# Kernel optimization log

Measured on AMD Instinct MI355X. Metric: run time of the kernel, lower is better.

## Reference

```python
import jax, jax.numpy as jnp
import numpy as np

B, S, E, D, DE = 8, 128, 50, 300, 50  # batch, seq, edge_dim, gcn_dim, dep_embed_dim
EPS = 1e-6


def setup_inputs() -> dict:
    key = jax.random.key(0)
    ks = jax.random.split(key, 9)
    weight_prob_softmax = jax.nn.softmax(jax.random.normal(ks[0], (B, S, S, E)), axis=2)
    weight_adj = jax.random.normal(ks[1], (B, S, S, E))
    gcn_inputs = jax.random.normal(ks[2], (B, S, D))
    # self-loop added to adjacency after permute -> [B, E, S, S]; identity loops
    self_loop = jnp.broadcast_to(jnp.eye(S, dtype=jnp.float32), (B, E, S, S))
    W_w = jax.random.normal(ks[3], (D, D)) * 0.05          # gcn linear (in, out)
    W_b = jnp.zeros((D,))
    ln_a = jnp.ones((D,))
    ln_b = jnp.zeros((D,))
    refine_W = jax.random.normal(ks[4], (2 * D + 3 * E, DE)) * 0.05  # (750, 50)
    refine_b = jnp.zeros((DE,))
    return {
        "weight_prob_softmax": weight_prob_softmax,
        "weight_adj": weight_adj,
        "gcn_inputs": gcn_inputs,
        "self_loop": self_loop,
        "W_w": W_w, "W_b": W_b,
        "ln_a": ln_a, "ln_b": ln_b,
        "refine_W": refine_W, "refine_b": refine_b,
    }


def reference(weight_prob_softmax, weight_adj, gcn_inputs, self_loop,
              W_w, W_b, ln_a, ln_b, refine_W, refine_b):
    b, s, d = gcn_inputs.shape
    e = weight_prob_softmax.shape[-1]
    # [B,S,S,E] -> [B,E,S,S], add self loops
    wps = jnp.transpose(weight_prob_softmax, (0, 3, 1, 2)) + self_loop
    # per-relation-channel message passing: Ax[b,e,i,:] = sum_j wps[b,e,i,j] * x[b,j,:]
    Ax = jnp.einsum('beij,bjd->beid', wps, gcn_inputs)
    Ax = Ax.mean(axis=1)  # avg pooling over edge channels -> [B,S,D]
    h = Ax @ W_w + W_b
    # LayerNorm with unbiased std (torch x.std default) and (std + eps)
    mean = h.mean(axis=-1, keepdims=True)
    var_unbiased = jnp.sum((h - mean) ** 2, axis=-1, keepdims=True) / (d - 1)
    std = jnp.sqrt(var_unbiased)
    h = ln_a * (h - mean) / (std + EPS) + ln_b
    node = jax.nn.relu(h)  # [B,S,D]
    # node1[b,i,j] = node[b,j]; node2[b,i,j] = node[b,i]
    node1 = jnp.broadcast_to(node[:, None, :, :], (b, s, s, d))
    node2 = jnp.broadcast_to(node[:, :, None, :], (b, s, s, d))
    # diagonal edge features: [B,E,S] -> [B,S,E]
    diag = jnp.transpose(jnp.diagonal(weight_adj, axis1=1, axis2=2), (0, 2, 1))
    edge_i = jnp.broadcast_to(diag[:, None, :, :], (b, s, s, e))  # edge_i[b,i,j]=diag[b,j]
    edge_j = jnp.broadcast_to(diag[:, :, None, :], (b, s, s, e))  # edge_j[b,i,j]=diag[b,i]
    feat = jnp.concatenate([weight_adj, edge_i, edge_j, node1, node2], axis=-1)
    edge_out = feat @ refine_W + refine_b  # [B,S,S,DE]
    return node, edge_out
```

## Files before the change

### kernel.cpp

```cpp
#include <hip/hip_runtime.h>
#include <hip/hip_bf16.h>


typedef __bf16 bf16x8 __attribute__((ext_vector_type(8)));
typedef float f32x4 __attribute__((ext_vector_type(4)));

__device__ __forceinline__ unsigned short f2bf(float f) {
    __hip_bfloat16 h = __float2bfloat16(f);
    union { __hip_bfloat16 h; unsigned short u; } c; c.h = h; return c.u;
}

__global__ void __launch_bounds__(512) k_node(
    const float* __restrict__ wps,
    const float* __restrict__ wa,
    const float* __restrict__ x,
    const float* __restrict__ Ww,
    const float* __restrict__ Wb,
    const float* __restrict__ lna,
    const float* __restrict__ lnb,
    const float* __restrict__ Rw,
    const float* __restrict__ rb,
    float* __restrict__ node_out,
    float* __restrict__ R1, float* __restrict__ R2)
{
    __shared__ __align__(16) float stageF[12800];
    __shared__ float Ml[4][128];
    __shared__ float axm[4][304];
    __shared__ float hl[4][304];
    __shared__ float diag[4][52];
    __shared__ float stats[8];
    int tid = threadIdx.x;
    int b = blockIdx.x >> 5;
    int ig = blockIdx.x & 31;
    int row0 = b * 128 + ig * 4;

    const float4* wb4 = (const float4*)(wps + (size_t)row0 * 6400);
    float4* s4 = (float4*)stageF;
    for (int c = 0; c < 2; ++c) {
        for (int i4 = tid; i4 < 3200; i4 += 512) s4[i4] = wb4[c * 3200 + i4];
        __syncthreads();
        if (tid < 256) {
            int rl = tid >> 7, j = tid & 127;
            const float* p = stageF + (rl * 128 + j) * 50;
            float s = 0.f;
#pragma unroll
            for (int e = 0; e < 50; e += 2) s += p[e] + p[e + 1];
            int r = c * 2 + rl;
            Ml[r][j] = s * (1.0f / 50.0f) + (((ig * 4 + r) == j) ? 1.0f : 0.0f);
        }
        __syncthreads();
    }
    if (tid < 200) {
        int r = tid / 50, e = tid % 50;
        diag[r][e] = wa[(((size_t)(row0 + r)) * 128 + (ig * 4 + r)) * 50 + e];
    }

    if (tid < 300) {
        float a0 = 0.f, a1 = 0.f, a2 = 0.f, a3 = 0.f;
        const float* xp = x + (size_t)b * 38400 + tid;
#pragma unroll 4
        for (int j = 0; j < 128; ++j) {
            float xv = xp[j * 300];
            a0 += Ml[0][j] * xv; a1 += Ml[1][j] * xv;
            a2 += Ml[2][j] * xv; a3 += Ml[3][j] * xv;
        }
        axm[0][tid] = a0; axm[1][tid] = a1; axm[2][tid] = a2; axm[3][tid] = a3;
    }
    __syncthreads();

    if (tid < 300) {
        float wb = Wb[tid];
        float h0 = wb, h1 = wb, h2 = wb, h3 = wb;
        const float* wp = Ww + tid;
#pragma unroll 4
        for (int k = 0; k < 300; ++k) {
            float w = wp[k * 300];
            h0 += axm[0][k] * w; h1 += axm[1][k] * w;
            h2 += axm[2][k] * w; h3 += axm[3][k] * w;
        }
        hl[0][tid] = h0; hl[1][tid] = h1; hl[2][tid] = h2; hl[3][tid] = h3;
    }
    __syncthreads();

    if (tid < 256) {
        int wv = tid >> 6, lane = tid & 63;
        float s1 = 0.f, s2 = 0.f;
        for (int dd = lane; dd < 300; dd += 64) {
            float v = hl[wv][dd]; s1 += v; s2 += v * v;
        }
        for (int off = 32; off > 0; off >>= 1) {
            s1 += __shfl_down(s1, off);
            s2 += __shfl_down(s2, off);
        }
        if (lane == 0) {
            float mean = s1 * (1.0f / 300.0f);
            float var = (s2 - 300.0f * mean * mean) * (1.0f / 299.0f);
            var = fmaxf(var, 0.0f);
            stats[wv * 2] = mean;
            stats[wv * 2 + 1] = 1.0f / (sqrtf(var) + 1e-6f);
        }
    }
    __syncthreads();
    if (tid < 300) {
        float la = lna[tid], lb = lnb[tid];
#pragma unroll
        for (int r = 0; r < 4; ++r) {
            float v = la * (hl[r][tid] - stats[r * 2]) * stats[r * 2 + 1] + lb;
            v = fmaxf(v, 0.0f);
            node_out[(size_t)(row0 + r) * 300 + tid] = v;
            axm[r][tid] = v;
        }
    }
    __syncthreads();

    if (tid < 400) {
        int k = tid % 50, p = tid / 50;
        float r1a[4] = {0.f, 0.f, 0.f, 0.f};
        float r2a[4] = {0.f, 0.f, 0.f, 0.f};
        int i0 = p * 44, i1 = (i0 + 44 < 350) ? i0 + 44 : 350;
        for (int idx = i0; idx < i1; ++idx) {
            float w1, w2;
            if (idx < 50) { w1 = Rw[(50 + idx) * 50 + k]; w2 = Rw[(100 + idx) * 50 + k]; }
            else { int d = idx - 50; w1 = Rw[(150 + d) * 50 + k]; w2 = Rw[(450 + d) * 50 + k]; }
#pragma unroll
            for (int r = 0; r < 4; ++r) {
                float m = (idx < 50) ? diag[r][idx] : axm[r][idx - 50];
                r1a[r] += m * w1; r2a[r] += m * w2;
            }
        }
#pragma unroll
        for (int r = 0; r < 4; ++r) {
            stageF[p * 200 + r * 50 + k] = r1a[r];
            stageF[1600 + p * 200 + r * 50 + k] = r2a[r];
        }
    }
    __syncthreads();
    if (tid < 200) {
        int r = tid / 50, k = tid % 50;
        float r1 = 0.f, r2 = rb[k];
#pragma unroll
        for (int p = 0; p < 8; ++p) {
            r1 += stageF[p * 200 + r * 50 + k];
            r2 += stageF[1600 + p * 200 + r * 50 + k];
        }
        R1[(size_t)(row0 + r) * 50 + k] = r1;
        R2[(size_t)(row0 + r) * 50 + k] = r2;
    }
}

__global__ void __launch_bounds__(256) k_edge(
    const float* __restrict__ wa,
    const float* __restrict__ Rw,
    const float* __restrict__ R1, const float* __restrict__ R2,
    float* __restrict__ eout)
{
    __shared__ __align__(16) unsigned char smem[27648];
    unsigned short* waA  = (unsigned short*)smem;
    unsigned short* rwBT = (unsigned short*)(smem + 18432);
    float* outF = (float*)smem;
    int tid = threadIdx.x;
    int bi = blockIdx.x;
    int b = bi >> 7;

    for (int idx = tid; idx < 2304; idx += 256) ((unsigned int*)rwBT)[idx] = 0u;
    for (int idx = tid; idx < 1408; idx += 256) {
        int j = idx / 11, c = idx % 11;
        *((unsigned int*)(waA + j * 72 + 50) + c) = 0u;
    }
    __syncthreads();

    const float2* wap = (const float2*)(wa + (size_t)bi * 6400);
    for (int idx = tid; idx < 3200; idx += 256) {
        float2 v = wap[idx];
        int f = idx * 2;
        int j = f / 50, e = f % 50;
        unsigned int pack = (unsigned int)f2bf(v.x) | ((unsigned int)f2bf(v.y) << 16);
        *(unsigned int*)(waA + j * 72 + e) = pack;
    }
    for (int idx = tid; idx < 2500; idx += 256) {
        int e = idx / 50, kk = idx % 50;
        rwBT[kk * 72 + e] = f2bf(Rw[idx]);
    }
    __syncthreads();

    int lane = tid & 63, wv = tid >> 6;
    int q = lane >> 4, lr = lane & 15;
    f32x4 acc[2][4] = {};

#pragma unroll
    for (int ks = 0; ks < 2; ++ks) {
        int e0 = ks * 32 + q * 8;
        bf16x8 a0 = *(const bf16x8*)&waA[(wv * 32 + lr) * 72 + e0];
        bf16x8 a1 = *(const bf16x8*)&waA[(wv * 32 + 16 + lr) * 72 + e0];
#pragma unroll
        for (int nt = 0; nt < 4; ++nt) {
            bf16x8 bb = *(const bf16x8*)&rwBT[(nt * 16 + lr) * 72 + e0];
            acc[0][nt] = __builtin_amdgcn_mfma_f32_16x16x32_bf16(a0, bb, acc[0][nt], 0, 0, 0);
            acc[1][nt] = __builtin_amdgcn_mfma_f32_16x16x32_bf16(a1, bb, acc[1][nt], 0, 0, 0);
        }
    }
    __syncthreads();

    const float* r2p = R2 + (size_t)bi * 50;
#pragma unroll
    for (int nt = 0; nt < 4; ++nt) {
        int kk = nt * 16 + lr;
        if (kk < 50) {
            float r2v = r2p[kk];
#pragma unroll
            for (int mi = 0; mi < 2; ++mi) {
                int jbase = wv * 32 + mi * 16 + q * 4;
#pragma unroll
                for (int r = 0; r < 4; ++r)
                    outF[(jbase + r) * 50 + kk] = acc[mi][nt][r] + r2v;
            }
        }
    }
    __syncthreads();

    const float4* R1b = (const float4*)(R1 + (size_t)b * 6400);
    const float4* L4  = (const float4*)outF;
    float4* op4 = (float4*)(eout + (size_t)bi * 6400);
    for (int f4 = tid; f4 < 1600; f4 += 256) {
        float4 v = L4[f4];
        float4 r = R1b[f4];
        v.x += r.x; v.y += r.y; v.z += r.z; v.w += r.w;
        op4[f4] = v;
    }
}

extern "C" void kernel_launch(void* const* d_in, const int* in_sizes, int n_in,
                              void* d_out, int out_size, void* d_ws, size_t ws_size,
                              hipStream_t stream)
{
    const float* wps = (const float*)d_in[0];
    const float* wa  = (const float*)d_in[1];
    const float* x   = (const float*)d_in[2];
    const float* Ww  = (const float*)d_in[4];
    const float* Wb  = (const float*)d_in[5];
    const float* lna = (const float*)d_in[6];
    const float* lnb = (const float*)d_in[7];
    const float* Rw  = (const float*)d_in[8];
    const float* rb  = (const float*)d_in[9];

    float* R1 = (float*)d_ws;
    float* R2 = ((float*)d_ws) + 51200;

    float* node_out = (float*)d_out;
    float* edge_out = node_out + 307200;

    k_node<<<256, 512, 0, stream>>>(wps, wa, x, Ww, Wb, lna, lnb, Rw, rb,
                                    node_out, R1, R2);
    k_edge<<<1024, 256, 0, stream>>>(wa, Rw, R1, R2, edge_out);
}
```

Baseline: 184.3 us.

## Precompute X·W once per batch and reassociate node aggregation

Reassociates (M·X)·W into M·(X·W): a new kernel computes X·W for all rows once, so each node block only does a 128-length aggregation instead of separate 128- and 300-length matmuls. The per-row edge-channel mean is now read directly from global memory without a shared staging pass, and the diag-dependent refine partial sums are computed by otherwise idle threads alongside the aggregation. It adds a third launch and uses the edge_out buffer as scratch for XW, which is safe only because k_edge overwrites it afterwards.

```diff
diff --git a/kernel.cpp b/kernel.cpp
--- a/kernel.cpp
+++ b/kernel.cpp
@@ -10,11 +10,37 @@
     union { __hip_bfloat16 h; unsigned short u; } c; c.h = h; return c.u;
 }
 
+__global__ void __launch_bounds__(320) k_xw(
+    const float* __restrict__ x, const float* __restrict__ Ww,
+    float* __restrict__ XW)
+{
+    __shared__ __align__(16) float xr[304];
+    int tid = threadIdx.x;
+    int row = blockIdx.x;
+    if (tid < 300) xr[tid] = x[(size_t)row * 300 + tid];
+    else if (tid < 304) xr[tid] = 0.f;
+    __syncthreads();
+    if (tid < 300) {
+        const float* wp = Ww + tid;
+        const f32x4* x4 = (const f32x4*)xr;
+        float acc = 0.f;
+#pragma unroll 5
+        for (int k4 = 0; k4 < 75; ++k4) {
+            f32x4 xv = x4[k4];
+            int k = k4 * 4;
+            acc += xv[0] * wp[(k + 0) * 300];
+            acc += xv[1] * wp[(k + 1) * 300];
+            acc += xv[2] * wp[(k + 2) * 300];
+            acc += xv[3] * wp[(k + 3) * 300];
+        }
+        XW[(size_t)row * 300 + tid] = acc;
+    }
+}
+
 __global__ void __launch_bounds__(512) k_node(
     const float* __restrict__ wps,
     const float* __restrict__ wa,
-    const float* __restrict__ x,
-    const float* __restrict__ Ww,
+    const float* __restrict__ XW,
     const float* __restrict__ Wb,
     const float* __restrict__ lna,
     const float* __restrict__ lnb,
@@ -23,62 +49,63 @@
     float* __restrict__ node_out,
     float* __restrict__ R1, float* __restrict__ R2)
 {
-    __shared__ __align__(16) float stageF[12800];
-    __shared__ float Ml[4][128];
-    __shared__ float axm[4][304];
+    __shared__ __align__(16) float Ml[128][4];
     __shared__ float hl[4][304];
+    __shared__ float nodeL[4][304];
     __shared__ float diag[4][52];
     __shared__ float stats[8];
+    __shared__ float part1[14][200];
+    __shared__ float part2[14][200];
     int tid = threadIdx.x;
     int b = blockIdx.x >> 5;
     int ig = blockIdx.x & 31;
     int row0 = b * 128 + ig * 4;
 
-    const float4* wb4 = (const float4*)(wps + (size_t)row0 * 6400);
-    float4* s4 = (float4*)stageF;
-    for (int c = 0; c < 2; ++c) {
-        for (int i4 = tid; i4 < 3200; i4 += 512) s4[i4] = wb4[c * 3200 + i4];
-        __syncthreads();
-        if (tid < 256) {
-            int rl = tid >> 7, j = tid & 127;
-            const float* p = stageF + (rl * 128 + j) * 50;
-            float s = 0.f;
-#pragma unroll
-            for (int e = 0; e < 50; e += 2) s += p[e] + p[e + 1];
-            int r = c * 2 + rl;
-            Ml[r][j] = s * (1.0f / 50.0f) + (((ig * 4 + r) == j) ? 1.0f : 0.0f);
-        }
-        __syncthreads();
-    }
     if (tid < 200) {
         int r = tid / 50, e = tid % 50;
         diag[r][e] = wa[(((size_t)(row0 + r)) * 128 + (ig * 4 + r)) * 50 + e];
     }
-
-    if (tid < 300) {
-        float a0 = 0.f, a1 = 0.f, a2 = 0.f, a3 = 0.f;
-        const float* xp = x + (size_t)b * 38400 + tid;
-#pragma unroll 4
-        for (int j = 0; j < 128; ++j) {
-            float xv = xp[j * 300];
-            a0 += Ml[0][j] * xv; a1 += Ml[1][j] * xv;
-            a2 += Ml[2][j] * xv; a3 += Ml[3][j] * xv;
-        }
-        axm[0][tid] = a0; axm[1][tid] = a1; axm[2][tid] = a2; axm[3][tid] = a3;
+    {
+        int r = tid >> 7, j = tid & 127;
+        const float2* p = (const float2*)(wps + ((size_t)(row0 + r)) * 6400 + j * 50);
+        float s = 0.f;
+#pragma unroll
+        for (int n = 0; n < 25; ++n) { float2 v = p[n]; s += v.x + v.y; }
+        Ml[j][r] = s * (1.0f / 50.0f) + (((ig * 4 + r) == j) ? 1.0f : 0.0f);
     }
     __syncthreads();
 
     if (tid < 300) {
         float wb = Wb[tid];
         float h0 = wb, h1 = wb, h2 = wb, h3 = wb;
-        const float* wp = Ww + tid;
-#pragma unroll 4
-        for (int k = 0; k < 300; ++k) {
-            float w = wp[k * 300];
-            h0 += axm[0][k] * w; h1 += axm[1][k] * w;
-            h2 += axm[2][k] * w; h3 += axm[3][k] * w;
+        const float* xwp = XW + (size_t)b * 38400 + tid;
+        const f32x4* M4 = (const f32x4*)Ml;
+#pragma unroll 16
+        for (int j = 0; j < 128; ++j) {
+            float xv = xwp[j * 300];
+            f32x4 m = M4[j];
+            h0 += m[0] * xv; h1 += m[1] * xv; h2 += m[2] * xv; h3 += m[3] * xv;
         }
         hl[0][tid] = h0; hl[1][tid] = h1; hl[2][tid] = h2; hl[3][tid] = h3;
+    } else if (tid >= 312) {
+        int t = tid - 312, p = t / 50, k = t % 50;
+        int e0 = p * 13, e1 = (e0 + 13 < 50) ? e0 + 13 : 50;
+        float r1a[4] = {0.f, 0.f, 0.f, 0.f};
+        float r2a[4] = {0.f, 0.f, 0.f, 0.f};
+        for (int e = e0; e < e1; ++e) {
+            float w1 = Rw[(50 + e) * 50 + k];
+            float w2 = Rw[(100 + e) * 50 + k];
+#pragma unroll
+            for (int r = 0; r < 4; ++r) {
+                r1a[r] += diag[r][e] * w1;
+                r2a[r] += diag[r][e] * w2;
+            }
+        }
+#pragma unroll
+        for (int r = 0; r < 4; ++r) {
+            part1[p][r * 50 + k] = r1a[r];
+            part2[p][r * 50 + k] = r2a[r];
+        }
     }
     __syncthreads();
 
@@ -101,6 +128,7 @@
         }
     }
     __syncthreads();
+
     if (tid < 300) {
         float la = lna[tid], lb = lnb[tid];
 #pragma unroll
@@ -108,43 +136,44 @@
             float v = la * (hl[r][tid] - stats[r * 2]) * stats[r * 2 + 1] + lb;
             v = fmaxf(v, 0.0f);
             node_out[(size_t)(row0 + r) * 300 + tid] = v;
-            axm[r][tid] = v;
-        }
-    }
-    __syncthreads();
-
-    if (tid < 400) {
-        int k = tid % 50, p = tid / 50;
+            nodeL[r][tid] = v;
+        }
+    }
+    __syncthreads();
+
+    if (tid < 500) {
+        int p = tid / 50, k = tid % 50;
+        int d0 = p * 30;
         float r1a[4] = {0.f, 0.f, 0.f, 0.f};
         float r2a[4] = {0.f, 0.f, 0.f, 0.f};
-        int i0 = p * 44, i1 = (i0 + 44 < 350) ? i0 + 44 : 350;
-        for (int idx = i0; idx < i1; ++idx) {
-            float w1, w2;
-            if (idx < 50) { w1 = Rw[(50 + idx) * 50 + k]; w2 = Rw[(100 + idx) * 50 + k]; }
-            else { int d = idx - 50; w1 = Rw[(150 + d) * 50 + k]; w2 = Rw[(450 + d) * 50 + k]; }
+#pragma unroll 6
+        for (int d = d0; d < d0 + 30; ++d) {
+            float w1 = Rw[(150 + d) * 50 + k];
+            float w2 = Rw[(450 + d) * 50 + k];
 #pragma unroll
             for (int r = 0; r < 4; ++r) {
-                float m = (idx < 50) ? diag[r][idx] : axm[r][idx - 50];
-                r1a[r] += m * w1; r2a[r] += m * w2;
+                r1a[r] += nodeL[r][d] * w1;
+                r2a[r] += nodeL[r][d] * w2;
             }
         }
 #pragma unroll
         for (int r = 0; r < 4; ++r) {
-            stageF[p * 200 + r * 50 + k] = r1a[r];
-            stageF[1600 + p * 200 + r * 50 + k] = r2a[r];
-        }
-    }
-    __syncthreads();
+            part1[4 + p][r * 50 + k] = r1a[r];
+            part2[4 + p][r * 50 + k] = r2a[r];
+        }
+    }
+    __syncthreads();
+
     if (tid < 200) {
         int r = tid / 50, k = tid % 50;
-        float r1 = 0.f, r2 = rb[k];
-#pragma unroll
-        for (int p = 0; p < 8; ++p) {
-            r1 += stageF[p * 200 + r * 50 + k];
-            r2 += stageF[1600 + p * 200 + r * 50 + k];
-        }
-        R1[(size_t)(row0 + r) * 50 + k] = r1;
-        R2[(size_t)(row0 + r) * 50 + k] = r2;
+        float s1 = 0.f, s2 = rb[k];
+#pragma unroll
+        for (int p = 0; p < 14; ++p) {
+            s1 += part1[p][r * 50 + k];
+            s2 += part2[p][r * 50 + k];
+        }
+        R1[(size_t)(row0 + r) * 50 + k] = s1;
+        R2[(size_t)(row0 + r) * 50 + k] = s2;
     }
 }
 
@@ -248,8 +277,10 @@
 
     float* node_out = (float*)d_out;
     float* edge_out = node_out + 307200;
-
-    k_node<<<256, 512, 0, stream>>>(wps, wa, x, Ww, Wb, lna, lnb, Rw, rb,
+    float* XW = edge_out;
+
+    k_xw  <<<1024, 320, 0, stream>>>(x, Ww, XW);
+    k_node<<<256, 512, 0, stream>>>(wps, wa, XW, Wb, lna, lnb, Rw, rb,
                                     node_out, R1, R2);
     k_edge<<<1024, 256, 0, stream>>>(wa, Rw, R1, R2, edge_out);
 }
```

New measurement: 160.3 us. 1.15x faster.

## Split edge-channel mean into separate kernel and widen node kernel with split-K

Applied to the files above, without the earlier changes.

The channel-mean reduction over the softmax tensor moves out of the node kernel into its own grid-wide kernel, which writes a mean adjacency matrix to workspace. The node kernel now runs 1024 threads per block. It splits the aggregation and linear-layer reductions across four thread groups with vectorized float4 accumulation, and reduces LayerNorm statistics across five wavefronts. This is meant to spread the bandwidth-heavy wps read across many more threads and blocks, and to raise parallelism in the serial node stage. The cost is an extra kernel launch and a workspace round trip for M.

```diff
diff --git a/kernel.cpp b/kernel.cpp
--- a/kernel.cpp
+++ b/kernel.cpp
@@ -10,8 +10,20 @@
     union { __hip_bfloat16 h; unsigned short u; } c; c.h = h; return c.u;
 }
 
-__global__ void __launch_bounds__(512) k_node(
-    const float* __restrict__ wps,
+__global__ void __launch_bounds__(256) k_msum(
+    const float* __restrict__ wps, float* __restrict__ M)
+{
+    int gid = blockIdx.x * 256 + threadIdx.x;
+    const float2* p = (const float2*)(wps + (size_t)gid * 50);
+    float s = 0.f;
+#pragma unroll
+    for (int n = 0; n < 25; ++n) { float2 v = p[n]; s += v.x + v.y; }
+    int i = (gid >> 7) & 127, j = gid & 127;
+    M[gid] = s * (1.0f / 50.0f) + ((i == j) ? 1.0f : 0.0f);
+}
+
+__global__ void __launch_bounds__(1024) k_node(
+    const float* __restrict__ M,
     const float* __restrict__ wa,
     const float* __restrict__ x,
     const float* __restrict__ Ww,
@@ -23,128 +35,149 @@
     float* __restrict__ node_out,
     float* __restrict__ R1, float* __restrict__ R2)
 {
-    __shared__ __align__(16) float stageF[12800];
-    __shared__ float Ml[4][128];
-    __shared__ float axm[4][304];
-    __shared__ float hl[4][304];
-    __shared__ float diag[4][52];
-    __shared__ float stats[8];
+    __shared__ __align__(16) float axp[4864];
+    __shared__ __align__(16) float axm4[1216];
+    __shared__ __align__(16) float Mlt[512];
+    __shared__ __align__(16) float srcL[1408];
+    __shared__ float red1[20], red2[20], stats[8];
+
     int tid = threadIdx.x;
-    int b = blockIdx.x >> 5;
-    int ig = blockIdx.x & 31;
-    int row0 = b * 128 + ig * 4;
-
-    const float4* wb4 = (const float4*)(wps + (size_t)row0 * 6400);
-    float4* s4 = (float4*)stageF;
-    for (int c = 0; c < 2; ++c) {
-        for (int i4 = tid; i4 < 3200; i4 += 512) s4[i4] = wb4[c * 3200 + i4];
-        __syncthreads();
-        if (tid < 256) {
-            int rl = tid >> 7, j = tid & 127;
-            const float* p = stageF + (rl * 128 + j) * 50;
-            float s = 0.f;
-#pragma unroll
-            for (int e = 0; e < 50; e += 2) s += p[e] + p[e + 1];
-            int r = c * 2 + rl;
-            Ml[r][j] = s * (1.0f / 50.0f) + (((ig * 4 + r) == j) ? 1.0f : 0.0f);
-        }
-        __syncthreads();
-    }
-    if (tid < 200) {
-        int r = tid / 50, e = tid % 50;
-        diag[r][e] = wa[(((size_t)(row0 + r)) * 128 + (ig * 4 + r)) * 50 + e];
-    }
-
-    if (tid < 300) {
-        float a0 = 0.f, a1 = 0.f, a2 = 0.f, a3 = 0.f;
-        const float* xp = x + (size_t)b * 38400 + tid;
+    int g = tid >> 8, t = tid & 255;
+    int row0 = blockIdx.x * 4;
+    int b = row0 >> 7, i0 = row0 & 127;
+
+    if (tid < 512) {
+        int r = tid >> 7, j = tid & 127;
+        Mlt[j * 4 + r] = M[(size_t)(row0 + r) * 128 + j];
+    } else if (tid < 712) {
+        int idx = tid - 512, r = idx / 50, e = idx % 50;
+        srcL[e * 4 + r] = wa[((size_t)(row0 + r) * 128 + (i0 + r)) * 50 + e];
+    }
+    __syncthreads();
+
+    int d0 = t;
+    bool has2 = (t < 44);
+    int d1 = has2 ? 256 + t : 299;
+
+    {
+        f32x4 a0 = {0.f, 0.f, 0.f, 0.f}, a1 = {0.f, 0.f, 0.f, 0.f};
+        const float* xp = x + (size_t)b * 38400;
+        int j0 = g * 32;
+#pragma unroll 8
+        for (int jj = 0; jj < 32; ++jj) {
+            int j = j0 + jj;
+            f32x4 m4 = *(const f32x4*)&Mlt[j * 4];
+            float xv0 = xp[j * 300 + d0];
+            float xv1 = xp[j * 300 + d1];
+            a0 += m4 * xv0;
+            a1 += m4 * xv1;
+        }
+        *(f32x4*)&axp[d0 * 16 + g * 4] = a0;
+        if (has2) *(f32x4*)&axp[d1 * 16 + g * 4] = a1;
+    }
+    __syncthreads();
+    if (tid < 304) {
+        f32x4 s = {0.f, 0.f, 0.f, 0.f};
+        if (tid < 300)
+            s = *(f32x4*)&axp[tid * 16]     + *(f32x4*)&axp[tid * 16 + 4]
+              + *(f32x4*)&axp[tid * 16 + 8] + *(f32x4*)&axp[tid * 16 + 12];
+        *(f32x4*)&axm4[tid * 4] = s;
+    }
+    __syncthreads();
+
+    {
+        f32x4 h0 = {0.f, 0.f, 0.f, 0.f}, h1 = {0.f, 0.f, 0.f, 0.f};
+        int kb = g * 76, ke = (g == 3) ? 300 : g * 76 + 76;
 #pragma unroll 4
-        for (int j = 0; j < 128; ++j) {
-            float xv = xp[j * 300];
-            a0 += Ml[0][j] * xv; a1 += Ml[1][j] * xv;
-            a2 += Ml[2][j] * xv; a3 += Ml[3][j] * xv;
-        }
-        axm[0][tid] = a0; axm[1][tid] = a1; axm[2][tid] = a2; axm[3][tid] = a3;
-    }
-    __syncthreads();
-
-    if (tid < 300) {
-        float wb = Wb[tid];
-        float h0 = wb, h1 = wb, h2 = wb, h3 = wb;
-        const float* wp = Ww + tid;
-#pragma unroll 4
-        for (int k = 0; k < 300; ++k) {
-            float w = wp[k * 300];
-            h0 += axm[0][k] * w; h1 += axm[1][k] * w;
-            h2 += axm[2][k] * w; h3 += axm[3][k] * w;
-        }
-        hl[0][tid] = h0; hl[1][tid] = h1; hl[2][tid] = h2; hl[3][tid] = h3;
-    }
-    __syncthreads();
-
-    if (tid < 256) {
-        int wv = tid >> 6, lane = tid & 63;
+        for (int k = kb; k < ke; ++k) {
+            f32x4 m4 = *(const f32x4*)&axm4[k * 4];
+            float w0 = Ww[k * 300 + d0];
+            float w1 = Ww[k * 300 + d1];
+            h0 += m4 * w0;
+            h1 += m4 * w1;
+        }
+        *(f32x4*)&axp[d0 * 16 + g * 4] = h0;
+        if (has2) *(f32x4*)&axp[d1 * 16 + g * 4] = h1;
+    }
+    __syncthreads();
+
+    f32x4 hv = {0.f, 0.f, 0.f, 0.f};
+    int wv = tid >> 6, lane = tid & 63;
+    if (tid < 320) {
+        if (tid < 300) {
+            hv = *(f32x4*)&axp[tid * 16]     + *(f32x4*)&axp[tid * 16 + 4]
+               + *(f32x4*)&axp[tid * 16 + 8] + *(f32x4*)&axp[tid * 16 + 12];
+            hv += Wb[tid];
+        }
+        float s1r[4], s2r[4];
+#pragma unroll
+        for (int r = 0; r < 4; ++r) { s1r[r] = hv[r]; s2r[r] = hv[r] * hv[r]; }
+        for (int off = 32; off; off >>= 1) {
+#pragma unroll
+            for (int r = 0; r < 4; ++r) {
+                s1r[r] += __shfl_down(s1r[r], off);
+                s2r[r] += __shfl_down(s2r[r], off);
+            }
+        }
+        if (lane == 0) {
+#pragma unroll
+            for (int r = 0; r < 4; ++r) { red1[wv * 4 + r] = s1r[r]; red2[wv * 4 + r] = s2r[r]; }
+        }
+    }
+    __syncthreads();
+    if (tid < 4) {
         float s1 = 0.f, s2 = 0.f;
-        for (int dd = lane; dd < 300; dd += 64) {
-            float v = hl[wv][dd]; s1 += v; s2 += v * v;
-        }
-        for (int off = 32; off > 0; off >>= 1) {
-            s1 += __shfl_down(s1, off);
-            s2 += __shfl_down(s2, off);
-        }
-        if (lane == 0) {
-            float mean = s1 * (1.0f / 300.0f);
-            float var = (s2 - 300.0f * mean * mean) * (1.0f / 299.0f);
-            var = fmaxf(var, 0.0f);
-            stats[wv * 2] = mean;
-            stats[wv * 2 + 1] = 1.0f / (sqrtf(var) + 1e-6f);
-        }
-    }
-    __syncthreads();
+#pragma unroll
+        for (int w = 0; w < 5; ++w) { s1 += red1[w * 4 + tid]; s2 += red2[w * 4 + tid]; }
+        float mean = s1 * (1.0f / 300.0f);
+        float var = (s2 - 300.0f * mean * mean) * (1.0f / 299.0f);
+        var = fmaxf(var, 0.0f);
+        stats[tid * 2] = mean;
+        stats[tid * 2 + 1] = 1.0f / (sqrtf(var) + 1e-6f);
+    }
+    __syncthreads();
+
     if (tid < 300) {
         float la = lna[tid], lb = lnb[tid];
+        f32x4 nv;
 #pragma unroll
         for (int r = 0; r < 4; ++r) {
-            float v = la * (hl[r][tid] - stats[r * 2]) * stats[r * 2 + 1] + lb;
-            v = fmaxf(v, 0.0f);
+            float v = la * (hv[r] - stats[r * 2]) * stats[r * 2 + 1] + lb;
+            v = fmaxf(v, 0.f);
+            nv[r] = v;
             node_out[(size_t)(row0 + r) * 300 + tid] = v;
-            axm[r][tid] = v;
-        }
-    }
-    __syncthreads();
-
-    if (tid < 400) {
-        int k = tid % 50, p = tid / 50;
-        float r1a[4] = {0.f, 0.f, 0.f, 0.f};
-        float r2a[4] = {0.f, 0.f, 0.f, 0.f};
-        int i0 = p * 44, i1 = (i0 + 44 < 350) ? i0 + 44 : 350;
-        for (int idx = i0; idx < i1; ++idx) {
+        }
+        *(f32x4*)&srcL[(50 + tid) * 4] = nv;
+    }
+    __syncthreads();
+
+    if (tid < 500) {
+        int p = tid / 50, k = tid % 50;
+        f32x4 r1a = {0.f, 0.f, 0.f, 0.f}, r2a = {0.f, 0.f, 0.f, 0.f};
+        int ib = p * 35;
+#pragma unroll 5
+        for (int idx = ib; idx < ib + 35; ++idx) {
+            f32x4 sv = *(const f32x4*)&srcL[idx * 4];
             float w1, w2;
             if (idx < 50) { w1 = Rw[(50 + idx) * 50 + k]; w2 = Rw[(100 + idx) * 50 + k]; }
             else { int d = idx - 50; w1 = Rw[(150 + d) * 50 + k]; w2 = Rw[(450 + d) * 50 + k]; }
-#pragma unroll
-            for (int r = 0; r < 4; ++r) {
-                float m = (idx < 50) ? diag[r][idx] : axm[r][idx - 50];
-                r1a[r] += m * w1; r2a[r] += m * w2;
-            }
-        }
-#pragma unroll
-        for (int r = 0; r < 4; ++r) {
-            stageF[p * 200 + r * 50 + k] = r1a[r];
-            stageF[1600 + p * 200 + r * 50 + k] = r2a[r];
-        }
+            r1a += sv * w1;
+            r2a += sv * w2;
+        }
+        *(f32x4*)&axp[(p * 50 + k) * 4] = r1a;
+        *(f32x4*)&axp[2000 + (p * 50 + k) * 4] = r2a;
     }
     __syncthreads();
     if (tid < 200) {
         int r = tid / 50, k = tid % 50;
-        float r1 = 0.f, r2 = rb[k];
-#pragma unroll
-        for (int p = 0; p < 8; ++p) {
-            r1 += stageF[p * 200 + r * 50 + k];
-            r2 += stageF[1600 + p * 200 + r * 50 + k];
-        }
-        R1[(size_t)(row0 + r) * 50 + k] = r1;
-        R2[(size_t)(row0 + r) * 50 + k] = r2;
+        float s1 = 0.f, s2 = rb[k];
+#pragma unroll
+        for (int p = 0; p < 10; ++p) {
+            s1 += axp[(p * 50 + k) * 4 + r];
+            s2 += axp[2000 + (p * 50 + k) * 4 + r];
+        }
+        R1[(size_t)(row0 + r) * 50 + k] = s1;
+        R2[(size_t)(row0 + r) * 50 + k] = s2;
     }
 }
 
@@ -245,11 +278,13 @@
 
     float* R1 = (float*)d_ws;
     float* R2 = ((float*)d_ws) + 51200;
+    float* M  = ((float*)d_ws) + 102400;
 
     float* node_out = (float*)d_out;
     float* edge_out = node_out + 307200;
 
-    k_node<<<256, 512, 0, stream>>>(wps, wa, x, Ww, Wb, lna, lnb, Rw, rb,
-                                    node_out, R1, R2);
+    k_msum<<<512, 256, 0, stream>>>(wps, M);
+    k_node<<<256, 1024, 0, stream>>>(M, wa, x, Ww, Wb, lna, lnb, Rw, rb,
+                                     node_out, R1, R2);
     k_edge<<<1024, 256, 0, stream>>>(wa, Rw, R1, R2, edge_out);
 }
```

Measured after the change: 151.8 us. -17.7%, faster.
